# Optimization experiments

Measured on AMD Instinct MI355X. Metric: run time of the kernel, lower is better.

The kernel has to match this reference:

```python
import jax, jax.numpy as jnp
import numpy as np

N_NODES = 100000
N_EDGES = 600000
IN_DIM = 128
OUT_DIM = 64


def setup_inputs() -> dict:
    key = jax.random.key(0)
    k1, k2, k3, k4, k5 = jax.random.split(key, 5)
    x = jax.random.normal(k1, (N_NODES, IN_DIM), dtype=jnp.float32)
    edge_index = jax.random.randint(k2, (2, N_EDGES), 0, N_NODES, dtype=jnp.int64)
    edge_weight = jax.random.uniform(k3, (N_EDGES,), dtype=jnp.float32)
    W1 = jax.random.normal(k4, (IN_DIM, IN_DIM), dtype=jnp.float32) / np.sqrt(IN_DIM)
    b1 = jnp.zeros((IN_DIM,), dtype=jnp.float32)
    W2 = jax.random.normal(k5, (IN_DIM, OUT_DIM), dtype=jnp.float32) / np.sqrt(IN_DIM)
    b2 = jnp.zeros((OUT_DIM,), dtype=jnp.float32)
    return {"x": x, "edge_index": edge_index, "edge_weight": edge_weight,
            "W1": W1, "b1": b1, "W2": W2, "b2": b2}


def _spmm(edge_index, edge_weight, h):
    # out[dst] = sum_{e: dst(e)=dst} w_e * h[src(e)]  -- normalized adjacency SpMM
    src, dst = edge_index[0], edge_index[1]
    msg = h[src] * edge_weight[:, None]          # [E, D] gather + scale
    return jax.ops.segment_sum(msg, dst, num_segments=h.shape[0])  # [N, D]


def reference(x, edge_index, edge_weight, W1, b1, W2, b2):
    # Layer 1: GCNConv(in,in) -> ReLU (dropout is identity in eval mode)
    h = _spmm(edge_index, edge_weight, x @ W1) + b1
    h = jax.nn.relu(h)
    # Layer 2: GCNConv(in,out)
    out = _spmm(edge_index, edge_weight, h @ W2) + b2
    return out
```

## Files before the change

### kernel.cpp

```cpp
#include <hip/hip_runtime.h>

#define NN 100000
#define NE 600000
#define DIN 128
#define DOUT 64
#define SCAN_B 512
#define NBLK ((NN + SCAN_B - 1) / SCAN_B)
#define HIST_B ((NE + 255) / 256)
#define G1_BM 128
#define G1B ((NN + G1_BM - 1) / G1_BM)
#define G1HB ((NN + 63) / 64)
#define ZB ((NN + 255) / 256)
#define W1B (DIN * DIN / 256)
#define W2B (DIN * DOUT / 256)
#define XS_PITCH 136

typedef __attribute__((ext_vector_type(8))) short bf16x8;
typedef __attribute__((ext_vector_type(4))) short s16x4;
typedef __attribute__((ext_vector_type(4))) float f32x4;
typedef __attribute__((ext_vector_type(2))) float f32x2;

__device__ inline short f2bf(float f) {
  union { float f; unsigned u; } v; v.f = f;
  unsigned r = (v.u + 0x7FFF + ((v.u >> 16) & 1)) >> 16;
  return (short)r;
}
__device__ inline float bf2f(unsigned short u) {
  union { unsigned u; float f; } v; v.u = ((unsigned)u) << 16;
  return v.f;
}
__device__ inline unsigned char f2fp8(float f) {
  unsigned pk = __builtin_amdgcn_cvt_pk_fp8_f32(f, f, 0, false);
  return (unsigned char)(pk & 0xff);
}
__device__ inline void fma_fp8x16(uint4 q, float w, float* acc) {
  f32x2 f;
  f = __builtin_amdgcn_cvt_pk_f32_fp8(q.x, false); acc[0] += w * f[0];  acc[1] += w * f[1];
  f = __builtin_amdgcn_cvt_pk_f32_fp8(q.x, true);  acc[2] += w * f[0];  acc[3] += w * f[1];
  f = __builtin_amdgcn_cvt_pk_f32_fp8(q.y, false); acc[4] += w * f[0];  acc[5] += w * f[1];
  f = __builtin_amdgcn_cvt_pk_f32_fp8(q.y, true);  acc[6] += w * f[0];  acc[7] += w * f[1];
  f = __builtin_amdgcn_cvt_pk_f32_fp8(q.z, false); acc[8] += w * f[0];  acc[9] += w * f[1];
  f = __builtin_amdgcn_cvt_pk_f32_fp8(q.z, true);  acc[10] += w * f[0]; acc[11] += w * f[1];
  f = __builtin_amdgcn_cvt_pk_f32_fp8(q.w, false); acc[12] += w * f[0]; acc[13] += w * f[1];
  f = __builtin_amdgcn_cvt_pk_f32_fp8(q.w, true);  acc[14] += w * f[0]; acc[15] += w * f[1];
}

__global__ __launch_bounds__(256) void prep_kernel(int* __restrict__ cnt,
                                                   const float* __restrict__ W1,
                                                   short* __restrict__ w1t,
                                                   const float* __restrict__ W2,
                                                   short* __restrict__ w2t) {
  const int b = blockIdx.x, t = threadIdx.x;
  if (b < ZB) {
    int i = b * 256 + t;
    if (i < NN) cnt[i] = 0;
  } else if (b < ZB + W1B) {
    int i = (b - ZB) * 256 + t;
    int n = i >> 7, k = i & 127;
    w1t[i] = f2bf(W1[k * DIN + n]);
  } else {
    int i = (b - ZB - W1B) * 256 + t;
    int n = i >> 7, k = i & 127;
    w2t[i] = f2bf(W2[k * DOUT + n]);
  }
}

__global__ __launch_bounds__(256) void gemm1_hist_kernel(const int* __restrict__ ei,
                                                         int* __restrict__ cnt,
                                                         int* __restrict__ rank,
                                                         const float* __restrict__ x,
                                                         const short* __restrict__ w1t,
                                                         unsigned char* __restrict__ h0) {
  __shared__ short xs[64][XS_PITCH];
  const int t = threadIdx.x;
  const int row0 = blockIdx.x * 64;

  float4 xv[8];
#pragma unroll
  for (int i = 0; i < 8; ++i) {
    int f = t + i * 256;
    int r = f >> 5, c4 = f & 31;
    int gr = row0 + r;
    xv[i] = (gr < NN) ? *(const float4*)&x[(size_t)gr * DIN + c4 * 4]
                      : make_float4(0.f, 0.f, 0.f, 0.f);
  }

  for (int e = blockIdx.x * 256 + t; e < NE; e += G1HB * 256)
    rank[e] = atomicAdd(&cnt[ei[NE + e]], 1);

#pragma unroll
  for (int i = 0; i < 8; ++i) {
    int f = t + i * 256;
    int r = f >> 5, c4 = f & 31;
    s16x4 s;
    s.x = f2bf(xv[i].x); s.y = f2bf(xv[i].y); s.z = f2bf(xv[i].z); s.w = f2bf(xv[i].w);
    *(s16x4*)&xs[r][c4 * 4] = s;
  }
  __syncthreads();

  const int wave = t >> 6, lane = t & 63;
  const int nlane = lane & 15, quad = lane >> 4;
  const int mbase = wave * 16;
  f32x4 acc[8];
#pragma unroll
  for (int nt = 0; nt < 8; ++nt) acc[nt] = (f32x4){0.f, 0.f, 0.f, 0.f};

#pragma unroll
  for (int ks = 0; ks < 4; ++ks) {
    const int koff = ks * 32 + quad * 8;
    bf16x8 a = *(const bf16x8*)&xs[mbase + nlane][koff];
#pragma unroll
    for (int nt = 0; nt < 8; ++nt) {
      bf16x8 bfr = *(const bf16x8*)&w1t[(size_t)(nt * 16 + nlane) * DIN + koff];
      acc[nt] = __builtin_amdgcn_mfma_f32_16x16x32_bf16(a, bfr, acc[nt], 0, 0, 0);
    }
  }
#pragma unroll
  for (int nt = 0; nt < 8; ++nt)
#pragma unroll
    for (int rg = 0; rg < 4; ++rg) {
      int gr = row0 + mbase + quad * 4 + rg;
      if (gr < NN) h0[(size_t)gr * DIN + nt * 16 + nlane] = f2fp8(acc[nt][rg]);
    }
}

__global__ __launch_bounds__(512) void scan_local_kernel(const int* __restrict__ cnt,
                                                         int* __restrict__ row_ptr,
                                                         int* __restrict__ blk_sum) {
  __shared__ int s[512];
  const int b = blockIdx.x, t = threadIdx.x;
  const int i = b * 512 + t;
  int v = (i < NN) ? cnt[i] : 0;
  s[t] = v;
  __syncthreads();
  for (int off = 1; off < 512; off <<= 1) {
    int u = (t >= off) ? s[t - off] : 0;
    __syncthreads();
    s[t] += u;
    __syncthreads();
  }
  if (i < NN) row_ptr[i] = s[t] - v;
  if (t == 511) blk_sum[b] = s[511];
}

__global__ __launch_bounds__(512) void scan_add_kernel(int* __restrict__ row_ptr,
                                                       const int* __restrict__ blk_sum) {
  __shared__ int s[512];
  const int b = blockIdx.x, t = threadIdx.x;
  s[t] = (t < NBLK) ? blk_sum[t] : 0;
  __syncthreads();
  for (int off = 1; off < 512; off <<= 1) {
    int u = (t >= off) ? s[t - off] : 0;
    __syncthreads();
    s[t] += u;
    __syncthreads();
  }
  int off = (b > 0) ? s[b - 1] : 0;
  const int i = b * 512 + t;
  if (i < NN) row_ptr[i] += off;
  if (b == 0 && t == 0) row_ptr[NN] = NE;
}

__global__ __launch_bounds__(256) void scatter_kernel(const int* __restrict__ ei,
                                                      const float* __restrict__ ew,
                                                      const int* __restrict__ row_ptr,
                                                      const int* __restrict__ rank,
                                                      int2* __restrict__ ep) {
  int e = blockIdx.x * 256 + threadIdx.x;
  if (e >= NE) return;
  int src = ei[e];
  int dst = ei[NE + e];
  int pos = row_ptr[dst] + rank[e];
  ep[pos] = make_int2(src, __float_as_int(ew[e]));
}

__global__ __launch_bounds__(512) void spmm1_gemm2_kernel(const int* __restrict__ rp,
                                                          const int2* __restrict__ ep,
                                                          const unsigned char* __restrict__ h,
                                                          const float* __restrict__ b1,
                                                          const short* __restrict__ w2t,
                                                          short* __restrict__ h2) {
  __shared__ short xs[G1_BM][XS_PITCH];
  const int t = threadIdx.x;
  const int row0 = blockIdx.x * G1_BM;
  const int sub = t >> 3, lane8 = t & 7;
  float bb[16];
  *(float4*)&bb[0]  = *(const float4*)&b1[lane8 * 16];
  *(float4*)&bb[4]  = *(const float4*)&b1[lane8 * 16 + 4];
  *(float4*)&bb[8]  = *(const float4*)&b1[lane8 * 16 + 8];
  *(float4*)&bb[12] = *(const float4*)&b1[lane8 * 16 + 12];

#pragma unroll
  for (int batch = 0; batch < 2; ++batch) {
    const int r = batch * 64 + sub;
    const int row = row0 + r;
    float acc[16];
#pragma unroll
    for (int j = 0; j < 16; ++j) acc[j] = 0.f;
    if (row < NN) {
      const int b0 = rp[row], e1 = rp[row + 1];
      int i = b0;
      for (; i + 4 <= e1; i += 4) {
        int2 p0 = ep[i], p1 = ep[i + 1], p2 = ep[i + 2], p3 = ep[i + 3];
        uint4 q0 = *(const uint4*)&h[(size_t)p0.x * DIN + lane8 * 16];
        uint4 q1 = *(const uint4*)&h[(size_t)p1.x * DIN + lane8 * 16];
        uint4 q2 = *(const uint4*)&h[(size_t)p2.x * DIN + lane8 * 16];
        uint4 q3 = *(const uint4*)&h[(size_t)p3.x * DIN + lane8 * 16];
        fma_fp8x16(q0, __int_as_float(p0.y), acc);
        fma_fp8x16(q1, __int_as_float(p1.y), acc);
        fma_fp8x16(q2, __int_as_float(p2.y), acc);
        fma_fp8x16(q3, __int_as_float(p3.y), acc);
      }
      if (i + 2 <= e1) {
        int2 p0 = ep[i], p1 = ep[i + 1];
        uint4 q0 = *(const uint4*)&h[(size_t)p0.x * DIN + lane8 * 16];
        uint4 q1 = *(const uint4*)&h[(size_t)p1.x * DIN + lane8 * 16];
        fma_fp8x16(q0, __int_as_float(p0.y), acc);
        fma_fp8x16(q1, __int_as_float(p1.y), acc);
        i += 2;
      }
      if (i < e1) {
        int2 p0 = ep[i];
        uint4 q0 = *(const uint4*)&h[(size_t)p0.x * DIN + lane8 * 16];
        fma_fp8x16(q0, __int_as_float(p0.y), acc);
      }
    }
    bf16x8 o0, o1;
#pragma unroll
    for (int j = 0; j < 8; ++j) {
      o0[j] = f2bf(fmaxf(acc[j] + bb[j], 0.f));
      o1[j] = f2bf(fmaxf(acc[8 + j] + bb[8 + j], 0.f));
    }
    *(bf16x8*)&xs[r][lane8 * 16] = o0;
    *(bf16x8*)&xs[r][lane8 * 16 + 8] = o1;
  }
  __syncthreads();

  const int wave = t >> 6, lane = t & 63;
  const int nlane = lane & 15, quad = lane >> 4;
  const int mbase = wave * 16;
  f32x4 acc2[4];
#pragma unroll
  for (int nt = 0; nt < 4; ++nt) acc2[nt] = (f32x4){0.f, 0.f, 0.f, 0.f};
#pragma unroll
  for (int ks = 0; ks < 4; ++ks) {
    const int koff = ks * 32 + quad * 8;
    bf16x8 a0 = *(const bf16x8*)&xs[mbase + nlane][koff];
#pragma unroll
    for (int nt = 0; nt < 4; ++nt) {
      bf16x8 bfr = *(const bf16x8*)&w2t[(size_t)(nt * 16 + nlane) * DIN + koff];
      acc2[nt] = __builtin_amdgcn_mfma_f32_16x16x32_bf16(a0, bfr, acc2[nt], 0, 0, 0);
    }
  }
#pragma unroll
  for (int nt = 0; nt < 4; ++nt)
#pragma unroll
    for (int rg = 0; rg < 4; ++rg) {
      int gr = row0 + mbase + quad * 4 + rg;
      if (gr < NN) h2[(size_t)gr * DOUT + nt * 16 + nlane] = f2bf(acc2[nt][rg]);
    }
}

__global__ __launch_bounds__(256) void spmm2_kernel(const int* __restrict__ rp,
                                                    const int2* __restrict__ ep,
                                                    const short* __restrict__ h,
                                                    const float* __restrict__ bias,
                                                    float* __restrict__ out) {
  const int row = blockIdx.x * 32 + (threadIdx.x >> 3);
  const int lane = threadIdx.x & 7;
  if (row >= NN) return;
  const int b = rp[row], e = rp[row + 1];
  float acc[8];
#pragma unroll
  for (int j = 0; j < 8; ++j) acc[j] = 0.f;
  int i = b;
  for (; i + 4 <= e; i += 4) {
    int2 p0 = ep[i], p1 = ep[i + 1], p2 = ep[i + 2], p3 = ep[i + 3];
    bf16x8 v0 = *(const bf16x8*)&h[(size_t)p0.x * DOUT + lane * 8];
    bf16x8 v1 = *(const bf16x8*)&h[(size_t)p1.x * DOUT + lane * 8];
    bf16x8 v2 = *(const bf16x8*)&h[(size_t)p2.x * DOUT + lane * 8];
    bf16x8 v3 = *(const bf16x8*)&h[(size_t)p3.x * DOUT + lane * 8];
    float w0 = __int_as_float(p0.y), w1 = __int_as_float(p1.y);
    float w2 = __int_as_float(p2.y), w3 = __int_as_float(p3.y);
#pragma unroll
    for (int j = 0; j < 8; ++j)
      acc[j] += w0 * bf2f((unsigned short)v0[j]) + w1 * bf2f((unsigned short)v1[j]) +
                w2 * bf2f((unsigned short)v2[j]) + w3 * bf2f((unsigned short)v3[j]);
  }
  if (i + 2 <= e) {
    int2 p0 = ep[i], p1 = ep[i + 1];
    bf16x8 v0 = *(const bf16x8*)&h[(size_t)p0.x * DOUT + lane * 8];
    bf16x8 v1 = *(const bf16x8*)&h[(size_t)p1.x * DOUT + lane * 8];
    float w0 = __int_as_float(p0.y), w1 = __int_as_float(p1.y);
#pragma unroll
    for (int j = 0; j < 8; ++j)
      acc[j] += w0 * bf2f((unsigned short)v0[j]) + w1 * bf2f((unsigned short)v1[j]);
    i += 2;
  }
  if (i < e) {
    int2 p0 = ep[i];
    bf16x8 v0 = *(const bf16x8*)&h[(size_t)p0.x * DOUT + lane * 8];
    float w0 = __int_as_float(p0.y);
#pragma unroll
    for (int j = 0; j < 8; ++j) acc[j] += w0 * bf2f((unsigned short)v0[j]);
  }
#pragma unroll
  for (int j = 0; j < 8; ++j) acc[j] += bias[lane * 8 + j];
  *(float4*)&out[(size_t)row * DOUT + lane * 8] = make_float4(acc[0], acc[1], acc[2], acc[3]);
  *(float4*)&out[(size_t)row * DOUT + lane * 8 + 4] = make_float4(acc[4], acc[5], acc[6], acc[7]);
}

extern "C" void kernel_launch(void* const* d_in, const int* in_sizes, int n_in,
                              void* d_out, int out_size, void* d_ws, size_t ws_size,
                              hipStream_t stream) {
  const float* x  = (const float*)d_in[0];
  const int*   ei = (const int*)d_in[1];
  const float* ew = (const float*)d_in[2];
  const float* W1 = (const float*)d_in[3];
  const float* b1 = (const float*)d_in[4];
  const float* W2 = (const float*)d_in[5];
  const float* b2 = (const float*)d_in[6];
  float* out = (float*)d_out;

  char* p = (char*)d_ws;
  int*   cnt     = (int*)p;                 p += sizeof(int) * NN;
  int*   row_ptr = (int*)p;                 p += sizeof(int) * (NN + 4);
  int*   blk_sum = (int*)p;                 p += sizeof(int) * (NBLK + 4);
  int*   rank    = (int*)p;                 p += sizeof(int) * NE;
  int2*  ep      = (int2*)p;                p += sizeof(int2) * NE;
  short* w1t     = (short*)p;               p += sizeof(short) * DIN * DIN;
  short* w2t     = (short*)p;               p += sizeof(short) * DIN * DOUT;
  unsigned char* h0 = (unsigned char*)p;    p += (size_t)NN * DIN;
  short* h2      = (short*)p;

  prep_kernel<<<ZB + W1B + W2B, 256, 0, stream>>>(cnt, W1, w1t, W2, w2t);
  gemm1_hist_kernel<<<G1HB, 256, 0, stream>>>(ei, cnt, rank, x, w1t, h0);
  scan_local_kernel<<<NBLK, 512, 0, stream>>>(cnt, row_ptr, blk_sum);
  scan_add_kernel<<<NBLK, 512, 0, stream>>>(row_ptr, blk_sum);
  scatter_kernel<<<HIST_B, 256, 0, stream>>>(ei, ew, row_ptr, rank, ep);
  spmm1_gemm2_kernel<<<G1B, 512, 0, stream>>>(row_ptr, ep, h0, b1, w2t, h2);
  spmm2_kernel<<<(NN + 31) / 32, 256, 0, stream>>>(row_ptr, ep, h2, b2, out);
}
```

Before: 234.1 us.

## Build CSR with per-block partitioned LDS histograms instead of global atomics

```diff
diff --git a/kernel.cpp b/kernel.cpp
--- a/kernel.cpp
+++ b/kernel.cpp
@@ -4,13 +4,12 @@
 #define NE 600000
 #define DIN 128
 #define DOUT 64
-#define SCAN_B 512
-#define NBLK ((NN + SCAN_B - 1) / SCAN_B)
-#define HIST_B ((NE + 255) / 256)
+#define KPB 2048
+#define NBH ((NN + KPB - 1) / KPB)
+#define SAB ((NN + 512) / 512)
 #define G1_BM 128
 #define G1B ((NN + G1_BM - 1) / G1_BM)
-#define G1HB ((NN + 63) / 64)
-#define ZB ((NN + 255) / 256)
+#define GMB ((NN + 63) / 64)
 #define W1B (DIN * DIN / 256)
 #define W2B (DIN * DOUT / 256)
 #define XS_PITCH 136
@@ -45,55 +44,134 @@
   f = __builtin_amdgcn_cvt_pk_f32_fp8(q.w, true);  acc[14] += w * f[0]; acc[15] += w * f[1];
 }
 
-__global__ __launch_bounds__(256) void prep_kernel(int* __restrict__ cnt,
-                                                   const float* __restrict__ W1,
+__global__ __launch_bounds__(256) void prep_kernel(const float* __restrict__ W1,
                                                    short* __restrict__ w1t,
                                                    const float* __restrict__ W2,
                                                    short* __restrict__ w2t) {
   const int b = blockIdx.x, t = threadIdx.x;
-  if (b < ZB) {
+  if (b < W1B) {
     int i = b * 256 + t;
-    if (i < NN) cnt[i] = 0;
-  } else if (b < ZB + W1B) {
-    int i = (b - ZB) * 256 + t;
     int n = i >> 7, k = i & 127;
     w1t[i] = f2bf(W1[k * DIN + n]);
   } else {
-    int i = (b - ZB - W1B) * 256 + t;
+    int i = (b - W1B) * 256 + t;
     int n = i >> 7, k = i & 127;
     w2t[i] = f2bf(W2[k * DOUT + n]);
   }
 }
 
-__global__ __launch_bounds__(256) void gemm1_hist_kernel(const int* __restrict__ ei,
-                                                         int* __restrict__ cnt,
-                                                         int* __restrict__ rank,
-                                                         const float* __restrict__ x,
-                                                         const short* __restrict__ w1t,
-                                                         unsigned char* __restrict__ h0) {
+__global__ __launch_bounds__(512) void hist_scan_kernel(const int* __restrict__ ei,
+                                                        int* __restrict__ row_ptr,
+                                                        int* __restrict__ blk_sum) {
+  __shared__ int cntl[KPB];
+  __shared__ int ps[512];
+  const int t = threadIdx.x, b = blockIdx.x;
+  const int lo = b * KPB;
+#pragma unroll
+  for (int j = 0; j < 4; ++j) cntl[t + j * 512] = 0;
+  __syncthreads();
+
+  const int4* dstp = (const int4*)(ei + NE);
+  for (int e4 = t; e4 < NE / 4; e4 += 512) {
+    int4 d = dstp[e4];
+    int k;
+    k = d.x - lo; if ((unsigned)k < KPB) atomicAdd(&cntl[k], 1);
+    k = d.y - lo; if ((unsigned)k < KPB) atomicAdd(&cntl[k], 1);
+    k = d.z - lo; if ((unsigned)k < KPB) atomicAdd(&cntl[k], 1);
+    k = d.w - lo; if ((unsigned)k < KPB) atomicAdd(&cntl[k], 1);
+  }
+  __syncthreads();
+
+  int c0 = cntl[4 * t], c1 = cntl[4 * t + 1], c2 = cntl[4 * t + 2], c3 = cntl[4 * t + 3];
+  int s = c0 + c1 + c2 + c3;
+  ps[t] = s;
+  __syncthreads();
+  for (int off = 1; off < 512; off <<= 1) {
+    int u = (t >= off) ? ps[t - off] : 0;
+    __syncthreads();
+    ps[t] += u;
+    __syncthreads();
+  }
+  int ex = ps[t] - s;
+  cntl[4 * t] = ex;
+  cntl[4 * t + 1] = ex + c0;
+  cntl[4 * t + 2] = ex + c0 + c1;
+  cntl[4 * t + 3] = ex + c0 + c1 + c2;
+  if (t == 511) blk_sum[b] = ps[511];
+  __syncthreads();
+#pragma unroll
+  for (int j = 0; j < 4; ++j) {
+    int k = t + j * 512;
+    if (lo + k < NN) row_ptr[lo + k] = cntl[k];
+  }
+}
+
+__global__ __launch_bounds__(512) void scan_add_kernel(int* __restrict__ row_ptr,
+                                                       const int* __restrict__ blk_sum) {
+  __shared__ int s[64];
+  const int b = blockIdx.x, t = threadIdx.x;
+  if (t < 64) s[t] = (t < NBH) ? blk_sum[t] : 0;
+  __syncthreads();
+  for (int off = 1; off < 64; off <<= 1) {
+    int u = (t < 64 && t >= off) ? s[t - off] : 0;
+    __syncthreads();
+    if (t < 64) s[t] += u;
+    __syncthreads();
+  }
+  const int i = b * 512 + t;
+  if (i < NN) {
+    int hb = i >> 11;
+    row_ptr[i] += (hb > 0) ? s[hb - 1] : 0;
+  } else if (i == NN) {
+    row_ptr[i] = NE;
+  }
+}
+
+__global__ __launch_bounds__(512) void scatter_part_kernel(const int* __restrict__ ei,
+                                                           const float* __restrict__ ew,
+                                                           const int* __restrict__ row_ptr,
+                                                           int2* __restrict__ ep) {
+  __shared__ int pos[KPB];
+  const int t = threadIdx.x, b = blockIdx.x;
+  const int lo = b * KPB;
+#pragma unroll
+  for (int j = 0; j < 4; ++j) {
+    int k = t + j * 512;
+    pos[k] = (lo + k < NN) ? row_ptr[lo + k] : 0;
+  }
+  __syncthreads();
+
+  const int4* dstp = (const int4*)(ei + NE);
+  for (int e4 = t; e4 < NE / 4; e4 += 512) {
+    int4 d = dstp[e4];
+    int e = e4 * 4;
+    int k;
+    k = d.x - lo;
+    if ((unsigned)k < KPB) { int p = atomicAdd(&pos[k], 1); ep[p] = make_int2(ei[e], __float_as_int(ew[e])); }
+    k = d.y - lo;
+    if ((unsigned)k < KPB) { int p = atomicAdd(&pos[k], 1); ep[p] = make_int2(ei[e + 1], __float_as_int(ew[e + 1])); }
+    k = d.z - lo;
+    if ((unsigned)k < KPB) { int p = atomicAdd(&pos[k], 1); ep[p] = make_int2(ei[e + 2], __float_as_int(ew[e + 2])); }
+    k = d.w - lo;
+    if ((unsigned)k < KPB) { int p = atomicAdd(&pos[k], 1); ep[p] = make_int2(ei[e + 3], __float_as_int(ew[e + 3])); }
+  }
+}
+
+__global__ __launch_bounds__(256) void gemm1_kernel(const float* __restrict__ x,
+                                                    const short* __restrict__ w1t,
+                                                    unsigned char* __restrict__ h0) {
   __shared__ short xs[64][XS_PITCH];
   const int t = threadIdx.x;
   const int row0 = blockIdx.x * 64;
-
-  float4 xv[8];
 #pragma unroll
   for (int i = 0; i < 8; ++i) {
     int f = t + i * 256;
     int r = f >> 5, c4 = f & 31;
     int gr = row0 + r;
-    xv[i] = (gr < NN) ? *(const float4*)&x[(size_t)gr * DIN + c4 * 4]
-                      : make_float4(0.f, 0.f, 0.f, 0.f);
-  }
-
-  for (int e = blockIdx.x * 256 + t; e < NE; e += G1HB * 256)
-    rank[e] = atomicAdd(&cnt[ei[NE + e]], 1);
-
-#pragma unroll
-  for (int i = 0; i < 8; ++i) {
-    int f = t + i * 256;
-    int r = f >> 5, c4 = f & 31;
+    float4 v = (gr < NN) ? *(const float4*)&x[(size_t)gr * DIN + c4 * 4]
+                         : make_float4(0.f, 0.f, 0.f, 0.f);
     s16x4 s;
-    s.x = f2bf(xv[i].x); s.y = f2bf(xv[i].y); s.z = f2bf(xv[i].z); s.w = f2bf(xv[i].w);
+    s.x = f2bf(v.x); s.y = f2bf(v.y); s.z = f2bf(v.z); s.w = f2bf(v.w);
     *(s16x4*)&xs[r][c4 * 4] = s;
   }
   __syncthreads();
@@ -122,56 +200,6 @@
       int gr = row0 + mbase + quad * 4 + rg;
       if (gr < NN) h0[(size_t)gr * DIN + nt * 16 + nlane] = f2fp8(acc[nt][rg]);
     }
-}
-
-__global__ __launch_bounds__(512) void scan_local_kernel(const int* __restrict__ cnt,
-                                                         int* __restrict__ row_ptr,
-                                                         int* __restrict__ blk_sum) {
-  __shared__ int s[512];
-  const int b = blockIdx.x, t = threadIdx.x;
-  const int i = b * 512 + t;
-  int v = (i < NN) ? cnt[i] : 0;
-  s[t] = v;
-  __syncthreads();
-  for (int off = 1; off < 512; off <<= 1) {
-    int u = (t >= off) ? s[t - off] : 0;
-    __syncthreads();
-    s[t] += u;
-    __syncthreads();
-  }
-  if (i < NN) row_ptr[i] = s[t] - v;
-  if (t == 511) blk_sum[b] = s[511];
-}
-
-__global__ __launch_bounds__(512) void scan_add_kernel(int* __restrict__ row_ptr,
-                                                       const int* __restrict__ blk_sum) {
-  __shared__ int s[512];
-  const int b = blockIdx.x, t = threadIdx.x;
-  s[t] = (t < NBLK) ? blk_sum[t] : 0;
-  __syncthreads();
-  for (int off = 1; off < 512; off <<= 1) {
-    int u = (t >= off) ? s[t - off] : 0;
-    __syncthreads();
-    s[t] += u;
-    __syncthreads();
-  }
-  int off = (b > 0) ? s[b - 1] : 0;
-  const int i = b * 512 + t;
-  if (i < NN) row_ptr[i] += off;
-  if (b == 0 && t == 0) row_ptr[NN] = NE;
-}
-
-__global__ __launch_bounds__(256) void scatter_kernel(const int* __restrict__ ei,
-                                                      const float* __restrict__ ew,
-                                                      const int* __restrict__ row_ptr,
-                                                      const int* __restrict__ rank,
-                                                      int2* __restrict__ ep) {
-  int e = blockIdx.x * 256 + threadIdx.x;
-  if (e >= NE) return;
-  int src = ei[e];
-  int dst = ei[NE + e];
-  int pos = row_ptr[dst] + rank[e];
-  ep[pos] = make_int2(src, __float_as_int(ew[e]));
 }
 
 __global__ __launch_bounds__(512) void spmm1_gemm2_kernel(const int* __restrict__ rp,
@@ -323,21 +351,19 @@
   float* out = (float*)d_out;
 
   char* p = (char*)d_ws;
-  int*   cnt     = (int*)p;                 p += sizeof(int) * NN;
   int*   row_ptr = (int*)p;                 p += sizeof(int) * (NN + 4);
-  int*   blk_sum = (int*)p;                 p += sizeof(int) * (NBLK + 4);
-  int*   rank    = (int*)p;                 p += sizeof(int) * NE;
+  int*   blk_sum = (int*)p;                 p += sizeof(int) * 64;
   int2*  ep      = (int2*)p;                p += sizeof(int2) * NE;
   short* w1t     = (short*)p;               p += sizeof(short) * DIN * DIN;
   short* w2t     = (short*)p;               p += sizeof(short) * DIN * DOUT;
   unsigned char* h0 = (unsigned char*)p;    p += (size_t)NN * DIN;
   short* h2      = (short*)p;
 
-  prep_kernel<<<ZB + W1B + W2B, 256, 0, stream>>>(cnt, W1, w1t, W2, w2t);
-  gemm1_hist_kernel<<<G1HB, 256, 0, stream>>>(ei, cnt, rank, x, w1t, h0);
-  scan_local_kernel<<<NBLK, 512, 0, stream>>>(cnt, row_ptr, blk_sum);
-  scan_add_kernel<<<NBLK, 512, 0, stream>>>(row_ptr, blk_sum);
-  scatter_kernel<<<HIST_B, 256, 0, stream>>>(ei, ew, row_ptr, rank, ep);
+  prep_kernel<<<W1B + W2B, 256, 0, stream>>>(W1, w1t, W2, w2t);
+  hist_scan_kernel<<<NBH, 512, 0, stream>>>(ei, row_ptr, blk_sum);
+  scan_add_kernel<<<SAB, 512, 0, stream>>>(row_ptr, blk_sum);
+  scatter_part_kernel<<<NBH, 512, 0, stream>>>(ei, ew, row_ptr, ep);
+  gemm1_kernel<<<GMB, 256, 0, stream>>>(x, w1t, h0);
   spmm1_gemm2_kernel<<<G1B, 512, 0, stream>>>(row_ptr, ep, h0, b1, w2t, h2);
   spmm2_kernel<<<(NN + 31) / 32, 256, 0, stream>>>(row_ptr, ep, h2, b2, out);
 }
```

After: 615.8 us. +163.1%, slower.
